# Kernel tuning notes

Hardware: AMD Instinct MI355X
Metric: run time of the kernel (lower is better)

The kernel has to match this reference:

```python
import jax, jax.numpy as jnp
import numpy as np

K, D, N = 32, 128, 65536
EPS = 1e-6


def setup_inputs() -> dict:
    key = jax.random.key(0)
    k1, k2, k3 = jax.random.split(key, 3)
    x = jax.random.normal(k1, (N, D), dtype=jnp.float32)
    means = jax.random.normal(k2, (K, D), dtype=jnp.float32)
    # SPD covariances (original init is identity; use SPD perturbation so Cholesky is valid)
    B = jax.random.normal(k3, (K, D, D), dtype=jnp.float32) * 0.1
    covariances = jnp.einsum('kij,klj->kil', B, B) / D + jnp.eye(D, dtype=jnp.float32)
    weights = jnp.ones((K,), dtype=jnp.float32) / K
    return {"x": x, "means": means, "covariances": covariances, "weights": weights}


def reference(x, means, covariances, weights):
    d = x.shape[-1]
    cov = covariances + EPS * jnp.eye(d, dtype=x.dtype)          # [K,D,D]
    L = jnp.linalg.cholesky(cov)                                 # [K,D,D]
    diff = x[None, :, :] - means[:, None, :]                     # [K,N,D]
    # Mahalanobis via triangular solve: m = ||L^{-1}(x-mu)||^2
    sol = jax.scipy.linalg.solve_triangular(
        L, jnp.swapaxes(diff, 1, 2), lower=True)                 # [K,D,N]
    maha = jnp.sum(sol * sol, axis=1)                            # [K,N]
    half_logdet = jnp.sum(jnp.log(jnp.diagonal(L, axis1=1, axis2=2)), axis=1)  # [K]
    log_prob = (-0.5 * (d * jnp.log(2.0 * jnp.pi) + maha)
                - half_logdet[:, None])                          # [K,N]
    weighted = log_prob.T + jnp.log(weights)                     # [N,K]
    return jax.nn.logsumexp(weighted, axis=1)                    # [N]
```

## Files before the change

kernel.cpp:

```cpp
#include <hip/hip_runtime.h>
#include <hip/hip_bf16.h>
#include <math.h>

#define KCOMP 32
#define DDIM  128
#define NPTS  65536
#define GMM_EPS 1e-6f
#define SA 129
#define UFT 1280

typedef __attribute__((ext_vector_type(8)))  __bf16 bf16x8;
typedef __attribute__((ext_vector_type(16))) float  f32x16;

__device__ __forceinline__ unsigned short f2bf(float f){
  unsigned u = __builtin_bit_cast(unsigned, f);
  u = (u + 0x7FFFu + ((u >> 16) & 1u)) >> 16;
  return (unsigned short)u;
}
__device__ __forceinline__ float rlane(float v, int lsrc){
  return __builtin_bit_cast(float, __builtin_amdgcn_readlane(__builtin_bit_cast(int, v), lsrc));
}

__device__ __noinline__ float chol_inv32(float* __restrict__ Ab,
                                         float* __restrict__ Wb,
                                         const int c){
  float ar[32], lr[32], rd[32], s[32];
  #pragma unroll
  for(int i=0;i<32;i++) ar[i] = Ab[i*SA + c];
  float mydiag = 1.f;
  #pragma unroll
  for(int j=0;j<32;j++){
    float d   = rlane(ar[j], j);
    float rsd = rsqrtf(d);
    rd[j] = rsd;
    float Lcj  = ar[j]*rsd;
    lr[j] = (c>=j) ? Lcj : 0.f;
    if(c==j) mydiag = Lcj;
    float coef = Lcj*rsd;
    #pragma unroll
    for(int i=j+1;i<32;i++){
      float bij = rlane(ar[i], j);
      ar[i] = fmaf(-bij, coef, ar[i]);
    }
  }
  #pragma unroll
  for(int j=0;j<32;j++) Ab[c*SA + j] = lr[j];
  #pragma unroll
  for(int i=0;i<32;i++) s[i] = (i==c) ? 1.f : 0.f;
  #pragma unroll
  for(int j=0;j<32;j++){
    float vj = s[j]*rd[j];
    s[j] = vj;
    #pragma unroll
    for(int i=j+1;i<32;i++)
      s[i] = fmaf(-rlane(lr[j], i), vj, s[i]);
  }
  #pragma unroll
  for(int i=0;i<32;i++) Wb[i*SA + c] = s[i];
  return logf(mydiag);
}

__device__ __noinline__ void panel_unit(float* __restrict__ A, const float* __restrict__ W,
                                        int r0, int c0, int b, int ibl){
  const int b32=b*32;
  float acc[4][4]={};
  for(int kc=0;kc<32;kc+=4){
    float a_[4][4], b_[4][4];
    #pragma unroll
    for(int e=0;e<4;e++)
      #pragma unroll
      for(int g=0;g<4;g++){
        a_[e][g]=A[(32*ibl+r0+e)*SA + b32+kc+g];
        b_[e][g]=W[(b32+c0+e)*SA   + b32+kc+g];
      }
    #pragma unroll
    for(int e=0;e<4;e++)
      #pragma unroll
      for(int f=0;f<4;f++)
        acc[e][f]+=a_[e][0]*b_[f][0]+a_[e][1]*b_[f][1]
                  +a_[e][2]*b_[f][2]+a_[e][3]*b_[f][3];
  }
  #pragma unroll
  for(int e=0;e<4;e++)
    #pragma unroll
    for(int f=0;f<4;f++)
      A[(32*ibl+r0+e)*SA + b32+c0+f] = acc[e][f];
}

__device__ __noinline__ void syrk_unit(float* __restrict__ A,
                                       int r0, int c0, int b, int ui, int uj){
  const int b32=b*32;
  float acc[4][4]={};
  for(int kc=0;kc<32;kc+=4){
    float a_[4][4], b_[4][4];
    #pragma unroll
    for(int e=0;e<4;e++)
      #pragma unroll
      for(int g=0;g<4;g++){
        a_[e][g]=A[(32*ui+r0+e)*SA + b32+kc+g];
        b_[e][g]=A[(32*uj+c0+e)*SA + b32+kc+g];
      }
    #pragma unroll
    for(int e=0;e<4;e++)
      #pragma unroll
      for(int f=0;f<4;f++)
        acc[e][f]+=a_[e][0]*b_[f][0]+a_[e][1]*b_[f][1]
                  +a_[e][2]*b_[f][2]+a_[e][3]*b_[f][3];
  }
  #pragma unroll
  for(int e=0;e<4;e++)
    #pragma unroll
    for(int f=0;f<4;f++)
      A[(32*ui+r0+e)*SA+32*uj+c0+f] -= acc[e][f];
}

__device__ __noinline__ void tg_unit(const float* __restrict__ A, const float* __restrict__ W,
                                     float* __restrict__ T, int r0, int c0, int i, int j){
  float acc[4][4]={};
  #pragma unroll 1
  for(int p=j;p<i;p++){
    for(int kc=0;kc<32;kc+=4){
      float a_[4][4], b_[4][4];
      #pragma unroll
      for(int e=0;e<4;e++)
        #pragma unroll
        for(int g=0;g<4;g++){
          a_[e][g]=A[(32*i+r0+e)*SA + 32*p+kc+g];
          b_[e][g]=W[(32*p+kc+e)*SA + 32*j+c0+g];
        }
      #pragma unroll
      for(int e=0;e<4;e++)
        #pragma unroll
        for(int f=0;f<4;f++)
          acc[e][f]+=a_[e][0]*b_[0][f]+a_[e][1]*b_[1][f]
                    +a_[e][2]*b_[2][f]+a_[e][3]*b_[3][f];
    }
  }
  #pragma unroll
  for(int e=0;e<4;e++)
    #pragma unroll
    for(int f=0;f<4;f++)
      T[(r0+e)*33+c0+f]=acc[e][f];
}

__device__ __noinline__ void a2_unit(float* __restrict__ W, const float* __restrict__ T,
                                     int r0, int c0, int i, int j){
  float ac2[4][4]={};
  for(int kc=0;kc<32;kc+=4){
    float a_[4][4], b_[4][4];
    #pragma unroll
    for(int e=0;e<4;e++)
      #pragma unroll
      for(int g=0;g<4;g++){
        a_[e][g]=W[(32*i+r0+e)*SA + 32*i+kc+g];
        b_[e][g]=T[(kc+e)*33 + c0+g];
      }
    #pragma unroll
    for(int e=0;e<4;e++)
      #pragma unroll
      for(int f=0;f<4;f++)
        ac2[e][f]+=a_[e][0]*b_[0][f]+a_[e][1]*b_[1][f]
                  +a_[e][2]*b_[2][f]+a_[e][3]*b_[3][f];
  }
  #pragma unroll
  for(int e=0;e<4;e++)
    #pragma unroll
    for(int f=0;f<4;f++)
      W[(32*i+r0+e)*SA+32*j+c0+f] = -ac2[e][f];
}

__device__ __forceinline__ void pack_tile(const float* __restrict__ W,
                                          uint4* __restrict__ uf4, int tile, int l){
  int db = (tile<2)?0:((tile<6)?1:((tile<12)?2:3));
  int kc = tile - ((db==0)?0:((db==1)?2:((db==2)?6:12)));
  int row=db*32+(l&31), colb=kc*16+((l>>5)<<3);
  unsigned uu[4];
  #pragma unroll
  for(int h2=0;h2<4;h2++){
    unsigned lo=f2bf(W[row*SA+colb+2*h2]);
    unsigned hi=f2bf(W[row*SA+colb+2*h2+1]);
    uu[h2]=lo|(hi<<16);
  }
  uint4 wv; wv.x=uu[0]; wv.y=uu[1]; wv.z=uu[2]; wv.w=uu[3];
  uf4[tile*64 + l] = wv;
}

__global__ __launch_bounds__(256) void k_prep(const float* __restrict__ cov,
                                              const float* __restrict__ wts,
                                              const float* __restrict__ means,
                                              float* __restrict__ ws_c3,
                                              unsigned short* __restrict__ qfrag,
                                              unsigned short* __restrict__ ufrag){
  __shared__ float A[DDIM*SA];
  __shared__ float W[DDIM*SA];
  __shared__ float Tb[3*1056];
  __shared__ float muS[DDIM];
  __shared__ float mq[256];
  const int t=threadIdx.x, w=t>>6, l=t&63, k=blockIdx.x;
  const int r0=(l>>3)*4, c0=(l&7)*4;
  uint4* ufK = (uint4*)ufrag + (size_t)k*UFT;

  const float4* cv4 = (const float4*)(cov + (size_t)k*DDIM*DDIM);
  #pragma unroll
  for(int v=0; v<16; v++){
    int idx4 = t + 256*v; float4 f = cv4[idx4];
    int e = idx4*4; int i = e>>7; int j = e&127;
    float* d = &A[i*SA+j]; d[0]=f.x; d[1]=f.y; d[2]=f.z; d[3]=f.w;
  }
  for(int z=t; z<DDIM*SA; z+=256) W[z] = 0.f;
  if(t<DDIM) muS[t] = means[k*DDIM+t];
  __syncthreads();
  if(t<DDIM) A[t*SA+t] += GMM_EPS;
  __syncthreads();

  float hl = 0.f;
  if(w==0) hl += chol_inv32(&A[0], &W[0], l&31);
  __syncthreads();
  if(w==1)      panel_unit(A,W,r0,c0,0,1);
  else if(w==2) panel_unit(A,W,r0,c0,0,2);
  else if(w==3) panel_unit(A,W,r0,c0,0,3);
  __syncthreads();
  if(w==0)      syrk_unit(A,r0,c0,0,1,1);
  else if(w==1) syrk_unit(A,r0,c0,0,2,1);
  else if(w==2) syrk_unit(A,r0,c0,0,3,1);
  else          syrk_unit(A,r0,c0,0,2,2);
  __syncthreads();
  if(w==0)      hl += chol_inv32(&A[32*SA+32], &W[32*SA+32], l&31);
  else if(w==1) syrk_unit(A,r0,c0,0,3,2);
  else if(w==2) syrk_unit(A,r0,c0,0,3,3);
  __syncthreads();
  if(w==1)      panel_unit(A,W,r0,c0,1,2);
  else if(w==2) panel_unit(A,W,r0,c0,1,3);
  else if(w==3) tg_unit(A,W,&Tb[0],r0,c0,1,0);
  __syncthreads();
  if(w==0)      syrk_unit(A,r0,c0,1,2,2);
  else if(w==1) a2_unit(W,&Tb[0],r0,c0,1,0);
  else if(w==2) tg_unit(A,W,&Tb[1056],r0,c0,2,1);
  else          syrk_unit(A,r0,c0,1,3,2);
  __syncthreads();
  if(w==0)      hl += chol_inv32(&A[64*SA+64], &W[64*SA+64], l&31);
  else if(w==1) syrk_unit(A,r0,c0,1,3,3);
  else if(w==2) tg_unit(A,W,&Tb[0],r0,c0,2,0);
  __syncthreads();
  if(w==1)      panel_unit(A,W,r0,c0,2,3);
  else if(w==2) a2_unit(W,&Tb[0],r0,c0,2,0);
  else if(w==3) a2_unit(W,&Tb[1056],r0,c0,2,1);
  __syncthreads();
  if(w==0)      syrk_unit(A,r0,c0,2,3,3);
  else if(w==1) tg_unit(A,W,&Tb[0],r0,c0,3,0);
  else if(w==2) tg_unit(A,W,&Tb[1056],r0,c0,3,1);
  else          tg_unit(A,W,&Tb[2112],r0,c0,3,2);
  __syncthreads();
  if(w==0)      hl += chol_inv32(&A[96*SA+96], &W[96*SA+96], l&31);
  else if(w==1 || (w==2 && l<32)){
    int r = (w==1)? l : 64+l;
    float s=0.f;
    #pragma unroll 8
    for(int c=0;c<DDIM;c++) s += W[r*SA+c]*muS[c];
    mq[r]=s;
  }
  __syncthreads();
  if(w==1)      a2_unit(W,&Tb[0],r0,c0,3,0);
  else if(w==2) a2_unit(W,&Tb[1056],r0,c0,3,1);
  else if(w==3) a2_unit(W,&Tb[2112],r0,c0,3,2);
  __syncthreads();
  if(w==0){
    if(l<32){
      int r = 96+l;
      float s=0.f;
      #pragma unroll 8
      for(int c=0;c<DDIM;c++) s += W[r*SA+c]*muS[c];
      mq[r]=s;
    }
  } else {
    #pragma unroll
    for(int j=0;j<4;j++) pack_tile(W, ufK, (w-1)*4+j, l);
  }
  __syncthreads();
  if(t<128){
    float s=0.f;
    #pragma unroll 8
    for(int r=0;r<DDIM;r++) s += W[r*SA+t]*mq[r];
    mq[128+t]=s;
  } else if(w==2){
    #pragma unroll
    for(int j=0;j<4;j++) pack_tile(W, ufK, 12+j, l);
  } else {
    #pragma unroll
    for(int j=0;j<4;j++) pack_tile(W, ufK, 16+j, l);
  }
  __syncthreads();
  if(w==0){
    float hv = (l<32)? hl : 0.f;
    float p  = mq[l]*mq[l] + mq[l+64]*mq[l+64];
    #pragma unroll
    for(int off=32; off; off>>=1){ hv += __shfl_xor(hv,off); p += __shfl_xor(p,off); }
    if(l==0) ws_c3[k] = logf(wts[k]) - hv - 117.6241322f - 0.5f*p;
  } else if(w==1 && l<16){
    int tile=l>>1, half=l&1;
    const float* qq=&mq[128 + tile*16 + half*8];
    unsigned uu[4];
    #pragma unroll
    for(int h2=0;h2<4;h2++){
      unsigned lo=f2bf(qq[2*h2]), hi=f2bf(qq[2*h2+1]);
      uu[h2]=lo|(hi<<16);
    }
    uint4 wv; wv.x=uu[0]; wv.y=uu[1]; wv.z=uu[2]; wv.w=uu[3];
    ((uint4*)qfrag)[tile*64 + half*32 + k] = wv;
  }
}

#define MFMA_B(acc,u,xv) acc=__builtin_amdgcn_mfma_f32_32x32x16_bf16(__builtin_bit_cast(bf16x8,u),xv,acc,0,0,0)

__global__ __launch_bounds__(512,1) void k_main(const float* __restrict__ x,
                                                const uint4* __restrict__ uf,
                                                const uint4* __restrict__ qf,
                                                const float* __restrict__ ws_c3,
                                                float* __restrict__ out){
  __shared__ uint4 xs[4*8*64];
  __shared__ float lin[KCOMP*128];
  __shared__ float mahaS[4*8*128];
  __shared__ float c3s[KCOMP];
  const int t=threadIdx.x, lane=t&63, w=t>>6;
  const int qh=lane>>5, ln=lane&31;
  const size_t n0=(size_t)blockIdx.x*128;

  if(t<KCOMP) c3s[t]=ws_c3[t];

  {
    const float* xb = x + n0*DDIM;
    #pragma unroll
    for(int j=0;j<8;j++){
      int idx = j*512 + t;
      int n = idx & 127, d0 = (idx>>7)*4;
      float4 f = *(const float4*)(xb + (size_t)n*DDIM + d0);
      unsigned lo = f2bf(f.x) | (((unsigned)f2bf(f.y))<<16);
      unsigned hi = f2bf(f.z) | (((unsigned)f2bf(f.w))<<16);
      int tile=n>>5, lnn=n&31, c=d0>>4, qq=(d0>>3)&1, e4=d0&7;
      *(uint2*)((char*)xs + tile*8192 + c*1024 + qq*512 + lnn*16 + e4*2)
          = make_uint2(lo,hi);
    }
  }
  __syncthreads();

  if(w<4){
    f32x16 aq={};
    #pragma unroll
    for(int c=0;c<8;c++){
      uint4 qr = qf[c*64+lane];
      bf16x8 xq = __builtin_bit_cast(bf16x8, xs[w*512 + c*64 + lane]);
      MFMA_B(aq, qr, xq);
    }
    #pragma unroll
    for(int r=0;r<16;r++){
      int row=(r&3)+8*(r>>2)+4*qh;
      lin[row*128 + w*32 + ln] = -2.f*aq[r];
    }
  }

  #pragma unroll 1
  for(int iter=0;iter<4;iter++){
    const int k = iter*8 + w;
    uint4 ur[20];
    #pragma unroll
    for(int j=0;j<20;j++) ur[j]=uf[(size_t)k*UFT + j*64 + lane];

    #pragma unroll 1
    for(int tile=0;tile<4;tile++){
      bf16x8 xf[8];
      #pragma unroll
      for(int c=0;c<8;c++) xf[c]=__builtin_bit_cast(bf16x8, xs[tile*512 + c*64 + lane]);
      f32x16 a0={},a1={},a2={},a3={};
      #pragma unroll
      for(int c=0;c<2;c++) MFMA_B(a0, ur[c],    xf[c]);
      #pragma unroll
      for(int c=0;c<4;c++) MFMA_B(a1, ur[2+c],  xf[c]);
      #pragma unroll
      for(int c=0;c<6;c++) MFMA_B(a2, ur[6+c],  xf[c]);
      #pragma unroll
      for(int c=0;c<8;c++) MFMA_B(a3, ur[12+c], xf[c]);
      float p0=0.f,p1=0.f,p2=0.f,p3=0.f;
      #pragma unroll
      for(int r=0;r<16;r+=2){
        p0=fmaf(a0[r],a0[r],p0); p1=fmaf(a0[r+1],a0[r+1],p1);
        p2=fmaf(a1[r],a1[r],p2); p3=fmaf(a1[r+1],a1[r+1],p3);
        p0=fmaf(a2[r],a2[r],p0); p1=fmaf(a2[r+1],a2[r+1],p1);
        p2=fmaf(a3[r],a3[r],p2); p3=fmaf(a3[r+1],a3[r+1],p3);
      }
      float p=(p0+p1)+(p2+p3);
      p += __shfl_xor(p,32);
      if(qh==0) mahaS[iter*1024 + w*128 + tile*32 + ln] = p;
    }
  }
  __syncthreads();

  if(t<128){
    float m_run=-INFINITY, s_run=0.f;
    #pragma unroll 1
    for(int k3=0;k3<KCOMP;k3++){
      float a  = c3s[k3] - 0.5f*(mahaS[(k3>>3)*1024 + (k3&7)*128 + t] + lin[k3*128 + t]);
      float nm = fmaxf(m_run,a);
      s_run = s_run*__expf(m_run-nm)+__expf(a-nm);
      m_run = nm;
    }
    out[n0+t] = m_run + logf(s_run);
  }
}

extern "C" void kernel_launch(void* const* d_in, const int* in_sizes, int n_in,
                              void* d_out, int out_size, void* d_ws, size_t ws_size,
                              hipStream_t stream){
  const float* x   = (const float*)d_in[0];
  const float* mu  = (const float*)d_in[1];
  const float* cov = (const float*)d_in[2];
  const float* wts = (const float*)d_in[3];
  float* out = (float*)d_out;
  char*  ws  = (char*)d_ws;

  float*          wsC3 = (float*)ws;
  unsigned short* wsQF = (unsigned short*)(ws + 512);
  unsigned short* wsUF = (unsigned short*)(ws + 16384);

  k_prep<<<KCOMP, 256, 0, stream>>>(cov, wts, mu, wsC3, wsQF, wsUF);
  k_main<<<NPTS/128, 512, 0, stream>>>(x, (const uint4*)wsUF, (const uint4*)wsQF, wsC3, out);
}
```

Baseline: 174.2 us.

## Pre-convert x to bf16 MFMA layout in extra prep blocks overlapping Cholesky

Adds extra blocks to the prep kernel that convert x from fp32 into the bf16 fragment layout in workspace, running alongside the serial per-component Cholesky blocks on otherwise idle CUs. The main kernel then copies pre-packed bf16 tiles straight into shared memory instead of converting fp32 loads itself. This removes conversion and halves x bytes read in the main kernel, at the cost of an extra 16MB write and read through workspace. A fallback keeps the old path when the workspace is too small.

Result: slower. 179.0 us (+2.8%).

```diff
diff --git a/kernel.cpp b/kernel.cpp
--- a/kernel.cpp
+++ b/kernel.cpp
@@ -185,18 +185,40 @@
   uf4[tile*64 + l] = wv;
 }
 
+template<int CONV>
 __global__ __launch_bounds__(256) void k_prep(const float* __restrict__ cov,
                                               const float* __restrict__ wts,
                                               const float* __restrict__ means,
+                                              const float* __restrict__ xsrc,
                                               float* __restrict__ ws_c3,
                                               unsigned short* __restrict__ qfrag,
-                                              unsigned short* __restrict__ ufrag){
+                                              unsigned short* __restrict__ ufrag,
+                                              unsigned short* __restrict__ xws){
+  const int t=threadIdx.x;
+  if(CONV && (int)blockIdx.x >= KCOMP){
+    const int cb = (int)blockIdx.x - KCOMP;
+    const float* xb = xsrc + (size_t)cb*128*DDIM;
+    char* dst = (char*)xws + (size_t)cb*32768;
+    #pragma unroll 1
+    for(int j=0;j<16;j++){
+      int idx = j*256 + t;
+      int n = idx & 127, d0 = (idx>>7)*4;
+      float4 f = *(const float4*)(xb + (size_t)n*DDIM + d0);
+      unsigned lo = f2bf(f.x) | (((unsigned)f2bf(f.y))<<16);
+      unsigned hi = f2bf(f.z) | (((unsigned)f2bf(f.w))<<16);
+      int tile=n>>5, lnn=n&31, c=d0>>4, qq=(d0>>3)&1, e4=d0&7;
+      *(uint2*)(dst + tile*8192 + c*1024 + qq*512 + lnn*16 + e4*2)
+          = make_uint2(lo,hi);
+    }
+    return;
+  }
+
   __shared__ float A[DDIM*SA];
   __shared__ float W[DDIM*SA];
   __shared__ float Tb[3*1056];
   __shared__ float muS[DDIM];
   __shared__ float mq[256];
-  const int t=threadIdx.x, w=t>>6, l=t&63, k=blockIdx.x;
+  const int w=t>>6, l=t&63, k=blockIdx.x;
   const int r0=(l>>3)*4, c0=(l&7)*4;
   uint4* ufK = (uint4*)ufrag + (size_t)k*UFT;
 
@@ -312,10 +334,12 @@
 
 #define MFMA_B(acc,u,xv) acc=__builtin_amdgcn_mfma_f32_32x32x16_bf16(__builtin_bit_cast(bf16x8,u),xv,acc,0,0,0)
 
+template<int PRE>
 __global__ __launch_bounds__(512,1) void k_main(const float* __restrict__ x,
                                                 const uint4* __restrict__ uf,
                                                 const uint4* __restrict__ qf,
                                                 const float* __restrict__ ws_c3,
+                                                const uint4* __restrict__ xws,
                                                 float* __restrict__ out){
   __shared__ uint4 xs[4*8*64];
   __shared__ float lin[KCOMP*128];
@@ -327,7 +351,11 @@
 
   if(t<KCOMP) c3s[t]=ws_c3[t];
 
-  {
+  if(PRE){
+    const uint4* xg = xws + (size_t)blockIdx.x*2048;
+    #pragma unroll
+    for(int j=0;j<4;j++) xs[j*512+t] = xg[j*512+t];
+  } else {
     const float* xb = x + n0*DDIM;
     #pragma unroll
     for(int j=0;j<8;j++){
@@ -420,7 +448,16 @@
   float*          wsC3 = (float*)ws;
   unsigned short* wsQF = (unsigned short*)(ws + 512);
   unsigned short* wsUF = (unsigned short*)(ws + 16384);
-
-  k_prep<<<KCOMP, 256, 0, stream>>>(cov, wts, mu, wsC3, wsQF, wsUF);
-  k_main<<<NPTS/128, 512, 0, stream>>>(x, (const uint4*)wsUF, (const uint4*)wsQF, wsC3, out);
-}
+  unsigned short* wsXF = (unsigned short*)(ws + (1u<<20));
+
+  const size_t need = (1ull<<20) + (size_t)NPTS*DDIM*2;
+  if(ws_size >= need){
+    k_prep<1><<<KCOMP + NPTS/128, 256, 0, stream>>>(cov, wts, mu, x, wsC3, wsQF, wsUF, wsXF);
+    k_main<1><<<NPTS/128, 512, 0, stream>>>(x, (const uint4*)wsUF, (const uint4*)wsQF,
+                                            wsC3, (const uint4*)wsXF, out);
+  } else {
+    k_prep<0><<<KCOMP, 256, 0, stream>>>(cov, wts, mu, x, wsC3, wsQF, wsUF, nullptr);
+    k_main<0><<<NPTS/128, 512, 0, stream>>>(x, (const uint4*)wsUF, (const uint4*)wsQF,
+                                            wsC3, nullptr, out);
+  }
+}
```
